# Kernel tuning notes

Measured on AMD Instinct MI355X. Metric: run time of the kernel, lower is better.

The kernel has to match this reference:

```python
import jax, jax.numpy as jnp
import numpy as np

B, T, D, H, C = 256, 512, 64, 512, 1

def setup_inputs() -> dict:
    key = jax.random.key(0)
    ks = jax.random.split(key, 12)
    return {
        "x": jax.random.normal(ks[0], (B, T, D), jnp.float32),
        "w_ih_mu": jax.random.normal(ks[1], (D, 4 * H), jnp.float32) * 0.1,
        "w_ih_rho": jax.random.normal(ks[2], (D, 4 * H), jnp.float32) - 6.0,
        "eps_ih": jax.random.normal(ks[3], (D, 4 * H), jnp.float32),
        "w_hh_mu": jax.random.normal(ks[4], (H, 4 * H), jnp.float32) * 0.1,
        "w_hh_rho": jax.random.normal(ks[5], (H, 4 * H), jnp.float32) - 6.0,
        "eps_hh": jax.random.normal(ks[6], (H, 4 * H), jnp.float32),
        "b_mu": jax.random.normal(ks[7], (4 * H,), jnp.float32) * 0.1,
        "b_rho": jax.random.normal(ks[8], (4 * H,), jnp.float32) - 6.0,
        "eps_b": jax.random.normal(ks[9], (4 * H,), jnp.float32),
        "lin_w": jax.random.normal(ks[10], (C, H), jnp.float32) * 0.04,
        "lin_b": jax.random.normal(ks[11], (C,), jnp.float32) * 0.04,
    }

def _sample(mu, rho, eps):
    # blitz reparameterization: sigma = log1p(exp(rho))
    return mu + jnp.log1p(jnp.exp(rho)) * eps

def reference(x, w_ih_mu, w_ih_rho, eps_ih, w_hh_mu, w_hh_rho, eps_hh,
              b_mu, b_rho, eps_b, lin_w, lin_b):
    w_ih = _sample(w_ih_mu, w_ih_rho, eps_ih)
    w_hh = _sample(w_hh_mu, w_hh_rho, eps_hh)
    b = _sample(b_mu, b_rho, eps_b)

    # precompute input projections for all timesteps: [T, B, 4H]
    x_proj = jnp.einsum('btd,dg->tbg', x, w_ih) + b

    def step(carry, xp_t):
        h, c = carry
        gates = xp_t + h @ w_hh                      # [B, 4H]
        i, f, g, o = jnp.split(gates, 4, axis=-1)
        i = jax.nn.sigmoid(i)
        f = jax.nn.sigmoid(f)
        g = jnp.tanh(g)
        o = jax.nn.sigmoid(o)
        c = f * c + i * g
        h = o * jnp.tanh(c)
        return (h, c), None

    h0 = jnp.zeros((x.shape[0], w_hh.shape[0]), x.dtype)
    (h_last, _), _ = jax.lax.scan(step, (h0, h0), x_proj)
    # original takes outputs[:, -1, :] == last hidden state, then Linear
    return h_last @ lin_w.T + lin_b
```

## Files before the change

### kernel.cpp

```cpp
#include <hip/hip_runtime.h>

typedef unsigned short u16;
typedef unsigned long long u64;
typedef short v8s __attribute__((ext_vector_type(8)));
typedef float v4f __attribute__((ext_vector_type(4)));
typedef unsigned v2u __attribute__((ext_vector_type(2)));
typedef unsigned v4u __attribute__((ext_vector_type(4)));

#define Bb 256
#define Tt 512
#define Dd 64
#define Hh 512
#define G4 2048

#define NGROUP 16
#define NCHUNK 16
#define BT 16
#define HC 32
#define NCOL 128

#define WHH_S 520
#define WIH_S 72
#define SMEM_BYTES (NCOL*WHH_S*2 + NCOL*WIH_S*2)

#define MFMA(a,b,c) __builtin_amdgcn_mfma_f32_16x16x32_bf16((a),(b),(c),0,0,0)

#define SENT 0xFFFFFFFFu

__device__ __forceinline__ u16 f2bf(float f) {
  unsigned u = __float_as_uint(f);
  unsigned r = (u + 0x7fffu + ((u >> 16) & 1u)) >> 16;
  return (u16)r;
}
__device__ __forceinline__ float bf2f(u16 v) {
  return __uint_as_float(((unsigned)v) << 16);
}
__device__ __forceinline__ float sigm(float x) { return 1.0f / (1.0f + __expf(-x)); }
__device__ __forceinline__ float tanh_f(float x) {
  float a = fabsf(x);
  float e = __expf(-2.0f * a);
  float r = (1.0f - e) / (1.0f + e);
  return copysignf(r, x);
}
__device__ __forceinline__ float softplus_f(float x) { return log1pf(__expf(x)); }

__global__ void k_prep(const float* __restrict__ x, u16* __restrict__ x_bf,
                       u16* __restrict__ h_buf)
{
  int stride = gridDim.x * blockDim.x;
  int gid = blockIdx.x * blockDim.x + threadIdx.x;

  const int NS = (4 * Bb * Hh * 2 + 256 * 4) / 16;
  for (int i = gid; i < NS; i += stride)
    ((uint4*)h_buf)[i] = make_uint4(~0u, ~0u, ~0u, ~0u);

  const int N4 = Tt * Bb * Dd / 4;
  for (int i = gid; i < N4; i += stride) {
    int idx = i * 4;
    int t = idx >> 14;
    int rem = idx & 16383;
    int b = rem >> 6;
    int d = rem & 63;
    float4 v = *(const float4*)(x + (size_t)b * (Tt * Dd) + t * Dd + d);
    unsigned lo = (unsigned)f2bf(v.x) | ((unsigned)f2bf(v.y) << 16);
    unsigned hi = (unsigned)f2bf(v.z) | ((unsigned)f2bf(v.w) << 16);
    *(uint2*)(x_bf + idx) = make_uint2(lo, hi);
  }
}

template<bool FAST>
__device__ __forceinline__ void run_steps(
    const u16* const* WhP, const u16* const* WxP,
    const float (*bs)[4], const u16* __restrict__ x_bf,
    u16* __restrict__ h_buf, int bat, int j0, int wv, int q, int ko)
{
  float cc[4] = {0.f, 0.f, 0.f, 0.f};

  for (int t = 0; t < Tt; ++t) {
    v4f ac0 = {0.f,0.f,0.f,0.f}, ac1 = {0.f,0.f,0.f,0.f};
    v4f ac2 = {0.f,0.f,0.f,0.f}, ac3 = {0.f,0.f,0.f,0.f};

    {
      const u16* xb = x_bf + (size_t)t * (Bb * Dd) + bat * Dd + ko;
      #pragma unroll
      for (int ks = 0; ks < 2; ++ks) {
        v8s xf = *(const v8s*)(xb + ks * 32);
        ac0 = MFMA(*(const v8s*)(WxP[0] + ks * 32), xf, ac0);
        ac1 = MFMA(*(const v8s*)(WxP[1] + ks * 32), xf, ac1);
        ac2 = MFMA(*(const v8s*)(WxP[2] + ks * 32), xf, ac2);
        ac3 = MFMA(*(const v8s*)(WxP[3] + ks * 32), xf, ac3);
      }
    }

    if (t > 0) {
      const u16* hb = h_buf + (size_t)(t & 3) * (Bb * Hh) + bat * Hh + ko;
      unsigned done = 0;
      v4u buf[16];
      do {
        #pragma unroll
        for (int c = 0; c < 16; ++c)
          if (!(done & (1u << c)))
            asm volatile("global_load_dwordx4 %0, %1, off offset:%c2 sc0 sc1"
                         : "=v"(buf[c]) : "v"(hb), "i"(c * 64));
        asm volatile("s_waitcnt vmcnt(0)");
        unsigned ready = 0;
        #pragma unroll
        for (int c = 0; c < 16; ++c)
          if (!(done & (1u << c))) {
            asm volatile("" : "+v"(buf[c]));
            unsigned m0 = buf[c][0] > buf[c][1] ? buf[c][0] : buf[c][1];
            unsigned m1 = buf[c][2] > buf[c][3] ? buf[c][2] : buf[c][3];
            unsigned mx = m0 > m1 ? m0 : m1;
            int ok = (mx != SENT);
            if (__all(ok)) ready |= (1u << c);
          }
        #pragma unroll
        for (int c = 0; c < 16; ++c)
          if (ready & (1u << c)) {
            v8s hf = __builtin_bit_cast(v8s, buf[c]);
            ac0 = MFMA(*(const v8s*)(WhP[0] + c * 32), hf, ac0);
            ac1 = MFMA(*(const v8s*)(WhP[1] + c * 32), hf, ac1);
            ac2 = MFMA(*(const v8s*)(WhP[2] + c * 32), hf, ac2);
            ac3 = MFMA(*(const v8s*)(WhP[3] + c * 32), hf, ac3);
          }
        done |= ready;
      } while (done != 0xFFFFu);
    }

    {
      u16 hv[4];
      #pragma unroll
      for (int r = 0; r < 4; ++r) {
        float ig = sigm  (ac0[r] + bs[0][r]);
        float fg = sigm  (ac1[r] + bs[1][r]);
        float gg = tanh_f(ac2[r] + bs[2][r]);
        float og = sigm  (ac3[r] + bs[3][r]);
        cc[r] = fg * cc[r] + ig * gg;
        hv[r] = f2bf(og * tanh_f(cc[r]));
      }
      v2u qv;
      qv[0] = (unsigned)hv[0] | ((unsigned)hv[1] << 16);
      qv[1] = (unsigned)hv[2] | ((unsigned)hv[3] << 16);
      u16* hp = h_buf + (size_t)((t + 1) & 3) * (Bb * Hh) + bat * Hh
              + j0 + wv * 16 + q * 4;
      if constexpr (FAST)
        asm volatile("global_store_dwordx2 %0, %1, off sc0"
                     :: "v"(hp), "v"(qv) : "memory");
      else
        asm volatile("global_store_dwordx2 %0, %1, off sc0 sc1"
                     :: "v"(hp), "v"(qv) : "memory");
    }

    if (t > 0) {
      u16* cp = h_buf + (size_t)((t - 1) & 3) * (Bb * Hh) + bat * Hh
              + j0 + wv * 16 + q * 4;
      v2u sv; sv[0] = SENT; sv[1] = SENT;
      if constexpr (FAST)
        asm volatile("global_store_dwordx2 %0, %1, off sc0"
                     :: "v"(cp), "v"(sv) : "memory");
      else
        asm volatile("global_store_dwordx2 %0, %1, off sc0 sc1"
                     :: "v"(cp), "v"(sv) : "memory");
    }
  }
}

__global__ __launch_bounds__(128, 1) void lstm_main(
    const float* __restrict__ whh_mu, const float* __restrict__ whh_rho, const float* __restrict__ whh_eps,
    const float* __restrict__ wih_mu, const float* __restrict__ wih_rho, const float* __restrict__ wih_eps,
    const float* __restrict__ b_mu,  const float* __restrict__ b_rho,  const float* __restrict__ b_eps,
    const u16* __restrict__ x_bf, u16* __restrict__ h_buf)
{
  extern __shared__ char smem[];
  u16* w_hh_lds = (u16*)smem;
  u16* w_ih_lds = w_hh_lds + NCOL * WHH_S;

  const int tid = threadIdx.x;
  const int jrow  = blockIdx.x & 15;
  const int g     = ((jrow & 7) << 1) | (jrow >> 3);
  const int chunk = blockIdx.x >> 4;
  const int b0    = g * BT;
  const int j0    = chunk * HC;

  unsigned* xcd_arr = (unsigned*)(h_buf + 4 * Bb * Hh);

  unsigned myx;
  asm volatile("s_getreg_b32 %0, hwreg(HW_REG_XCC_ID)" : "=s"(myx));
  myx &= 0xffu;
  unsigned mv = 0x100u | myx;
  if (tid == 0) {
    unsigned* xp = xcd_arr + blockIdx.x;
    asm volatile("global_store_dword %0, %1, off sc0 sc1"
                 :: "v"(xp), "v"(mv) : "memory");
  }

  {
    const int lc = tid;
    const int gcol = (lc >> 5) * Hh + j0 + (lc & 31);
    #pragma unroll 4
    for (int k = 0; k < Hh; ++k) {
      int gi = k * G4 + gcol;
      float w = whh_mu[gi] + softplus_f(whh_rho[gi]) * whh_eps[gi];
      w_hh_lds[lc * WHH_S + k] = f2bf(w);
    }
    #pragma unroll 4
    for (int k = 0; k < Dd; ++k) {
      int gi = k * G4 + gcol;
      float w = wih_mu[gi] + softplus_f(wih_rho[gi]) * wih_eps[gi];
      w_ih_lds[lc * WIH_S + k] = f2bf(w);
    }
  }

  const int lane = tid & 63;
  const int wv   = tid >> 6;
  const int ln   = lane & 15;
  const int q    = lane >> 4;
  const int ko   = q * 8;

  const u16* WhP[4]; const u16* WxP[4];
  #pragma unroll
  for (int gt = 0; gt < 4; ++gt) {
    int rt = gt * 2 + wv;
    WhP[gt] = w_hh_lds + (rt * 16 + ln) * WHH_S + ko;
    WxP[gt] = w_ih_lds + (rt * 16 + ln) * WIH_S + ko;
  }

  const int bat = b0 + ln;

  float bs[4][4];
  #pragma unroll
  for (int gt = 0; gt < 4; ++gt)
    #pragma unroll
    for (int r = 0; r < 4; ++r) {
      int colg = gt * Hh + j0 + wv * 16 + q * 4 + r;
      bs[gt][r] = b_mu[colg] + softplus_f(b_rho[colg]) * b_eps[colg];
    }

  int fast;
  {
    const unsigned* xp = xcd_arr + (lane & 15) * 16 + jrow;
    for (;;) {
      unsigned v;
      asm volatile("global_load_dword %0, %1, off sc0 sc1"
                   : "=v"(v) : "v"(xp));
      asm volatile("s_waitcnt vmcnt(0)");
      asm volatile("" : "+v"(v));
      if (__all((int)(v != SENT))) {
        fast = __all((int)(v == mv));
        break;
      }
    }
  }

  __syncthreads();

  if (fast)
    run_steps<true >(WhP, WxP, bs, x_bf, h_buf, bat, j0, wv, q, ko);
  else
    run_steps<false>(WhP, WxP, bs, x_bf, h_buf, bat, j0, wv, q, ko);
}

__global__ void k_out(const u16* __restrict__ h, const float* __restrict__ lw,
                      const float* __restrict__ lb, float* __restrict__ out)
{
  int b = blockIdx.x * 64 + threadIdx.x;
  if (b >= Bb) return;
  const u16* hr = h + b * Hh;
  float acc = 0.f;
  #pragma unroll 8
  for (int k = 0; k < Hh; ++k) acc += bf2f(hr[k]) * lw[k];
  out[b] = acc + lb[0];
}

extern "C" void kernel_launch(void* const* d_in, const int* in_sizes, int n_in,
                              void* d_out, int out_size, void* d_ws, size_t ws_size,
                              hipStream_t stream)
{
  (void)in_sizes; (void)n_in; (void)out_size; (void)ws_size;
  const float* x       = (const float*)d_in[0];
  const float* wih_mu  = (const float*)d_in[1];
  const float* wih_rho = (const float*)d_in[2];
  const float* wih_eps = (const float*)d_in[3];
  const float* whh_mu  = (const float*)d_in[4];
  const float* whh_rho = (const float*)d_in[5];
  const float* whh_eps = (const float*)d_in[6];
  const float* b_mu    = (const float*)d_in[7];
  const float* b_rho   = (const float*)d_in[8];
  const float* b_eps   = (const float*)d_in[9];
  const float* lin_w   = (const float*)d_in[10];
  const float* lin_b   = (const float*)d_in[11];
  float* out = (float*)d_out;

  u16* x_bf  = (u16*)d_ws;
  u16* h_buf = x_bf + (size_t)Tt * Bb * Dd;

  k_prep<<<2048, 256, 0, stream>>>(x, x_bf, h_buf);

  hipFuncSetAttribute(reinterpret_cast<const void*>(lstm_main),
                      hipFuncAttributeMaxDynamicSharedMemorySize, SMEM_BYTES);
  lstm_main<<<NGROUP * NCHUNK, 128, SMEM_BYTES, stream>>>(
      whh_mu, whh_rho, whh_eps, wih_mu, wih_rho, wih_eps,
      b_mu, b_rho, b_eps, x_bf, h_buf);

  k_out<<<(Bb + 63) / 64, 64, 0, stream>>>(h_buf, lin_w, lin_b, out);
}
```

Before: 2.064 ms.

## Use one wave per block and issue x and h loads together

Each workgroup now runs a single 64-lane wave that computes all 8 gate row-tiles (both 16-column halves), instead of two waves splitting them. Each wave therefore polls the h buffer once per block rather than twice. The x-projection loads and the first round of h polling loads are now issued together up front, so the x MFMAs can overlap the latency of the cross-block h reads. The cost is twice the MFMA work and accumulator registers per wave, plus a longer serial weight-sampling prologue, on a latency-bound recurrent critical path.

New measurement: 3.414 ms. +65.4%, slower.

```diff
diff --git a/kernel.cpp b/kernel.cpp
--- a/kernel.cpp
+++ b/kernel.cpp
@@ -72,36 +72,59 @@
 __device__ __forceinline__ void run_steps(
     const u16* const* WhP, const u16* const* WxP,
     const float (*bs)[4], const u16* __restrict__ x_bf,
-    u16* __restrict__ h_buf, int bat, int j0, int wv, int q, int ko)
-{
-  float cc[4] = {0.f, 0.f, 0.f, 0.f};
+    u16* __restrict__ h_buf, int bat, int j0, int q, int ko)
+{
+  float cc[2][4] = {{0.f,0.f,0.f,0.f},{0.f,0.f,0.f,0.f}};
 
   for (int t = 0; t < Tt; ++t) {
-    v4f ac0 = {0.f,0.f,0.f,0.f}, ac1 = {0.f,0.f,0.f,0.f};
-    v4f ac2 = {0.f,0.f,0.f,0.f}, ac3 = {0.f,0.f,0.f,0.f};
-
+    v4f ac[8];
+    #pragma unroll
+    for (int i = 0; i < 8; ++i) ac[i] = v4f{0.f,0.f,0.f,0.f};
+
+    const u16* xb = x_bf + (size_t)t * (Bb * Dd) + bat * Dd + ko;
+    const u16* hb = h_buf + (size_t)(t & 3) * (Bb * Hh) + bat * Hh + ko;
+
+    v4u xv0, xv1;
+    v4u buf[16];
+    unsigned done = 0;
+
+    asm volatile("global_load_dwordx4 %0, %1, off"
+                 : "=v"(xv0) : "v"(xb));
+    asm volatile("global_load_dwordx4 %0, %1, off offset:64"
+                 : "=v"(xv1) : "v"(xb));
+    if (t > 0) {
+      #pragma unroll
+      for (int c = 0; c < 16; ++c)
+        asm volatile("global_load_dwordx4 %0, %1, off offset:%c2 sc0 sc1"
+                     : "=v"(buf[c]) : "v"(hb), "i"(c * 64));
+      asm volatile("s_waitcnt vmcnt(16)");
+    } else {
+      asm volatile("s_waitcnt vmcnt(0)");
+    }
+    asm volatile("" : "+v"(xv0));
+    asm volatile("" : "+v"(xv1));
     {
-      const u16* xb = x_bf + (size_t)t * (Bb * Dd) + bat * Dd + ko;
-      #pragma unroll
-      for (int ks = 0; ks < 2; ++ks) {
-        v8s xf = *(const v8s*)(xb + ks * 32);
-        ac0 = MFMA(*(const v8s*)(WxP[0] + ks * 32), xf, ac0);
-        ac1 = MFMA(*(const v8s*)(WxP[1] + ks * 32), xf, ac1);
-        ac2 = MFMA(*(const v8s*)(WxP[2] + ks * 32), xf, ac2);
-        ac3 = MFMA(*(const v8s*)(WxP[3] + ks * 32), xf, ac3);
-      }
+      v8s xf0 = __builtin_bit_cast(v8s, xv0);
+      v8s xf1 = __builtin_bit_cast(v8s, xv1);
+      #pragma unroll
+      for (int i = 0; i < 8; ++i)
+        ac[i] = MFMA(*(const v8s*)(WxP[i]), xf0, ac[i]);
+      #pragma unroll
+      for (int i = 0; i < 8; ++i)
+        ac[i] = MFMA(*(const v8s*)(WxP[i] + 32), xf1, ac[i]);
     }
 
     if (t > 0) {
-      const u16* hb = h_buf + (size_t)(t & 3) * (Bb * Hh) + bat * Hh + ko;
-      unsigned done = 0;
-      v4u buf[16];
+      bool first = true;
       do {
-        #pragma unroll
-        for (int c = 0; c < 16; ++c)
-          if (!(done & (1u << c)))
-            asm volatile("global_load_dwordx4 %0, %1, off offset:%c2 sc0 sc1"
-                         : "=v"(buf[c]) : "v"(hb), "i"(c * 64));
+        if (!first) {
+          #pragma unroll
+          for (int c = 0; c < 16; ++c)
+            if (!(done & (1u << c)))
+              asm volatile("global_load_dwordx4 %0, %1, off offset:%c2 sc0 sc1"
+                           : "=v"(buf[c]) : "v"(hb), "i"(c * 64));
+        }
+        first = false;
         asm volatile("s_waitcnt vmcnt(0)");
         unsigned ready = 0;
         #pragma unroll
@@ -118,31 +141,31 @@
         for (int c = 0; c < 16; ++c)
           if (ready & (1u << c)) {
             v8s hf = __builtin_bit_cast(v8s, buf[c]);
-            ac0 = MFMA(*(const v8s*)(WhP[0] + c * 32), hf, ac0);
-            ac1 = MFMA(*(const v8s*)(WhP[1] + c * 32), hf, ac1);
-            ac2 = MFMA(*(const v8s*)(WhP[2] + c * 32), hf, ac2);
-            ac3 = MFMA(*(const v8s*)(WhP[3] + c * 32), hf, ac3);
+            #pragma unroll
+            for (int i = 0; i < 8; ++i)
+              ac[i] = MFMA(*(const v8s*)(WhP[i] + c * 32), hf, ac[i]);
           }
         done |= ready;
       } while (done != 0xFFFFu);
     }
 
-    {
+    #pragma unroll
+    for (int half = 0; half < 2; ++half) {
       u16 hv[4];
       #pragma unroll
       for (int r = 0; r < 4; ++r) {
-        float ig = sigm  (ac0[r] + bs[0][r]);
-        float fg = sigm  (ac1[r] + bs[1][r]);
-        float gg = tanh_f(ac2[r] + bs[2][r]);
-        float og = sigm  (ac3[r] + bs[3][r]);
-        cc[r] = fg * cc[r] + ig * gg;
-        hv[r] = f2bf(og * tanh_f(cc[r]));
+        float ig = sigm  (ac[0*2+half][r] + bs[0*2+half][r]);
+        float fg = sigm  (ac[1*2+half][r] + bs[1*2+half][r]);
+        float gg = tanh_f(ac[2*2+half][r] + bs[2*2+half][r]);
+        float og = sigm  (ac[3*2+half][r] + bs[3*2+half][r]);
+        cc[half][r] = fg * cc[half][r] + ig * gg;
+        hv[r] = f2bf(og * tanh_f(cc[half][r]));
       }
       v2u qv;
       qv[0] = (unsigned)hv[0] | ((unsigned)hv[1] << 16);
       qv[1] = (unsigned)hv[2] | ((unsigned)hv[3] << 16);
       u16* hp = h_buf + (size_t)((t + 1) & 3) * (Bb * Hh) + bat * Hh
-              + j0 + wv * 16 + q * 4;
+              + j0 + half * 16 + q * 4;
       if constexpr (FAST)
         asm volatile("global_store_dwordx2 %0, %1, off sc0"
                      :: "v"(hp), "v"(qv) : "memory");
@@ -152,20 +175,23 @@
     }
 
     if (t > 0) {
-      u16* cp = h_buf + (size_t)((t - 1) & 3) * (Bb * Hh) + bat * Hh
-              + j0 + wv * 16 + q * 4;
-      v2u sv; sv[0] = SENT; sv[1] = SENT;
-      if constexpr (FAST)
-        asm volatile("global_store_dwordx2 %0, %1, off sc0"
-                     :: "v"(cp), "v"(sv) : "memory");
-      else
-        asm volatile("global_store_dwordx2 %0, %1, off sc0 sc1"
-                     :: "v"(cp), "v"(sv) : "memory");
-    }
-  }
-}
-
-__global__ __launch_bounds__(128, 1) void lstm_main(
+      #pragma unroll
+      for (int half = 0; half < 2; ++half) {
+        u16* cp = h_buf + (size_t)((t - 1) & 3) * (Bb * Hh) + bat * Hh
+                + j0 + half * 16 + q * 4;
+        v2u sv; sv[0] = SENT; sv[1] = SENT;
+        if constexpr (FAST)
+          asm volatile("global_store_dwordx2 %0, %1, off sc0"
+                       :: "v"(cp), "v"(sv) : "memory");
+        else
+          asm volatile("global_store_dwordx2 %0, %1, off sc0 sc1"
+                       :: "v"(cp), "v"(sv) : "memory");
+      }
+    }
+  }
+}
+
+__global__ __launch_bounds__(64, 1) void lstm_main(
     const float* __restrict__ whh_mu, const float* __restrict__ whh_rho, const float* __restrict__ whh_eps,
     const float* __restrict__ wih_mu, const float* __restrict__ wih_rho, const float* __restrict__ wih_eps,
     const float* __restrict__ b_mu,  const float* __restrict__ b_rho,  const float* __restrict__ b_eps,
@@ -194,8 +220,7 @@
                  :: "v"(xp), "v"(mv) : "memory");
   }
 
-  {
-    const int lc = tid;
+  for (int lc = tid; lc < NCOL; lc += 64) {
     const int gcol = (lc >> 5) * Hh + j0 + (lc & 31);
     #pragma unroll 4
     for (int k = 0; k < Hh; ++k) {
@@ -212,29 +237,29 @@
   }
 
   const int lane = tid & 63;
-  const int wv   = tid >> 6;
   const int ln   = lane & 15;
   const int q    = lane >> 4;
   const int ko   = q * 8;
 
-  const u16* WhP[4]; const u16* WxP[4];
+  const u16* WhP[8]; const u16* WxP[8];
   #pragma unroll
-  for (int gt = 0; gt < 4; ++gt) {
-    int rt = gt * 2 + wv;
-    WhP[gt] = w_hh_lds + (rt * 16 + ln) * WHH_S + ko;
-    WxP[gt] = w_ih_lds + (rt * 16 + ln) * WIH_S + ko;
+  for (int i = 0; i < 8; ++i) {
+    WhP[i] = w_hh_lds + (i * 16 + ln) * WHH_S + ko;
+    WxP[i] = w_ih_lds + (i * 16 + ln) * WIH_S + ko;
   }
 
   const int bat = b0 + ln;
 
-  float bs[4][4];
+  float bs[8][4];
   #pragma unroll
   for (int gt = 0; gt < 4; ++gt)
     #pragma unroll
-    for (int r = 0; r < 4; ++r) {
-      int colg = gt * Hh + j0 + wv * 16 + q * 4 + r;
-      bs[gt][r] = b_mu[colg] + softplus_f(b_rho[colg]) * b_eps[colg];
-    }
+    for (int half = 0; half < 2; ++half)
+      #pragma unroll
+      for (int r = 0; r < 4; ++r) {
+        int colg = gt * Hh + j0 + half * 16 + q * 4 + r;
+        bs[gt * 2 + half][r] = b_mu[colg] + softplus_f(b_rho[colg]) * b_eps[colg];
+      }
 
   int fast;
   {
@@ -255,9 +280,9 @@
   __syncthreads();
 
   if (fast)
-    run_steps<true >(WhP, WxP, bs, x_bf, h_buf, bat, j0, wv, q, ko);
+    run_steps<true >(WhP, WxP, bs, x_bf, h_buf, bat, j0, q, ko);
   else
-    run_steps<false>(WhP, WxP, bs, x_bf, h_buf, bat, j0, wv, q, ko);
+    run_steps<false>(WhP, WxP, bs, x_bf, h_buf, bat, j0, q, ko);
 }
 
 __global__ void k_out(const u16* __restrict__ h, const float* __restrict__ lw,
@@ -298,7 +323,7 @@
 
   hipFuncSetAttribute(reinterpret_cast<const void*>(lstm_main),
                       hipFuncAttributeMaxDynamicSharedMemorySize, SMEM_BYTES);
-  lstm_main<<<NGROUP * NCHUNK, 128, SMEM_BYTES, stream>>>(
+  lstm_main<<<NGROUP * NCHUNK, 64, SMEM_BYTES, stream>>>(
       whh_mu, whh_rho, whh_eps, wih_mu, wih_rho, wih_eps,
       b_mu, b_rho, b_eps, x_bf, h_buf);
 
```
